# Kernel optimization log

Measured on AMD Instinct MI355X. Metric: run time of the kernel, lower is better.

## Reference

```python
import jax, jax.numpy as jnp
import numpy as np

B, T_IN, T_OUT = 64, 512, 500
N_MEL, ENC_DIM, ATT_DIM = 80, 512, 128
ATT_RNN, DEC_RNN, PRENET = 1024, 1024, 256
N_FILT, KSIZE = 32, 31
PAD = (KSIZE - 1) // 2


def setup_inputs() -> dict:
    key = jax.random.key(0)
    ks = jax.random.split(key, 20)
    g = lambda i, shape, s: jax.random.normal(ks[i], shape, jnp.float32) * s
    return {
        'memory': g(0, (B, T_IN, ENC_DIM), 1.0),
        'decoder_inputs': g(1, (B, N_MEL, T_OUT), 1.0),
        'memory_lengths': jax.random.randint(ks[2], (B,), T_IN // 2, T_IN + 1).astype(jnp.int32),
        'prenet_w1': g(3, (PRENET, N_MEL), 0.05),
        'prenet_w2': g(4, (PRENET, PRENET), 0.05),
        'att_wih': g(5, (4 * ATT_RNN, PRENET + ENC_DIM), 0.02),
        'att_whh': g(6, (4 * ATT_RNN, ATT_RNN), 0.02),
        'att_bih': jnp.zeros((4 * ATT_RNN,), jnp.float32),
        'att_bhh': jnp.zeros((4 * ATT_RNN,), jnp.float32),
        'wq': g(7, (ATT_DIM, ATT_RNN), 0.03),
        'wm': g(8, (ATT_DIM, ENC_DIM), 0.03),
        'v': g(9, (ATT_DIM,), 0.05),
        'loc_conv': g(10, (N_FILT, 2, KSIZE), 0.05),
        'loc_dense': g(11, (ATT_DIM, N_FILT), 0.05),
        'dec_wih': g(12, (4 * DEC_RNN, ATT_RNN + ENC_DIM), 0.02),
        'dec_whh': g(13, (4 * DEC_RNN, DEC_RNN), 0.02),
        'dec_bih': jnp.zeros((4 * DEC_RNN,), jnp.float32),
        'dec_bhh': jnp.zeros((4 * DEC_RNN,), jnp.float32),
        'proj_w': g(14, (N_MEL, DEC_RNN + ENC_DIM), 0.02),
        'proj_b': jnp.zeros((N_MEL,), jnp.float32),
        'gate_w': g(15, (1, DEC_RNN + ENC_DIM), 0.02),
        'gate_b': jnp.zeros((1,), jnp.float32),
    }


def _lstm_cell(x, h, c, wih, whh, bih, bhh):
    gates = x @ wih.T + bih + h @ whh.T + bhh
    i, f, g, o = jnp.split(gates, 4, axis=-1)
    c_new = jax.nn.sigmoid(f) * c + jax.nn.sigmoid(i) * jnp.tanh(g)
    h_new = jax.nn.sigmoid(o) * jnp.tanh(c_new)
    return h_new, c_new


def _forward(memory, decoder_inputs, memory_lengths, prenet_w1, prenet_w2,
             att_wih, att_whh, att_bih, att_bhh, wq, wm, v, loc_conv, loc_dense,
             dec_wih, dec_whh, dec_bih, dec_bhh, proj_w, proj_b, gate_w, gate_b):
    # padding mask: True at padded encoder positions
    mask = jnp.arange(T_IN)[None, :] >= memory_lengths[:, None]  # [B, T_in]
    processed_memory = memory @ wm.T  # [B, T_in, ATT_DIM]

    # parse decoder inputs -> [T_out, B, N_MEL]; prepend all-zero go frame
    di = jnp.transpose(decoder_inputs, (2, 0, 1))
    di = jnp.concatenate([jnp.zeros((1, B, N_MEL), di.dtype), di], axis=0)

    # prenet (dropout p=0.5 is always active in the original; deterministic key)
    dk1, dk2 = jax.random.split(jax.random.key(42))
    x = jax.nn.relu(di @ prenet_w1.T)
    x = x * jax.random.bernoulli(dk1, 0.5, x.shape).astype(x.dtype) * 2.0
    x = jax.nn.relu(x @ prenet_w2.T)
    x = x * jax.random.bernoulli(dk2, 0.5, x.shape).astype(x.dtype) * 2.0  # [T_out+1, B, PRENET]

    def step(carry, x_t):
        ah, ac, dh, dc, aw, awc, ctx = carry
        # attention LSTM
        ah, ac = _lstm_cell(jnp.concatenate([x_t, ctx], -1), ah, ac,
                            att_wih, att_whh, att_bih, att_bhh)
        # location-sensitive attention
        awcat = jnp.stack([aw, awc], axis=1)  # [B, 2, T_in]
        loc = jax.lax.conv_general_dilated(awcat, loc_conv, (1,), [(PAD, PAD)],
                                           dimension_numbers=('NCH', 'OIH', 'NCH'))  # [B, F, T_in]
        loc = jnp.einsum('bft,af->bta', loc, loc_dense)  # [B, T_in, ATT_DIM]
        pq = (ah @ wq.T)[:, None, :]  # [B, 1, ATT_DIM]
        energies = jnp.tanh(pq + loc + processed_memory) @ v  # [B, T_in]
        energies = jnp.where(mask, -jnp.inf, energies)
        aw = jax.nn.softmax(energies, axis=1)
        ctx = jnp.einsum('bt,btd->bd', aw, memory)
        awc = awc + aw
        # decoder LSTM
        dh, dc = _lstm_cell(jnp.concatenate([ah, ctx], -1), dh, dc,
                            dec_wih, dec_whh, dec_bih, dec_bhh)
        dhc = jnp.concatenate([dh, ctx], -1)  # [B, DEC_RNN+ENC_DIM]
        mel = dhc @ proj_w.T + proj_b  # [B, N_MEL]
        gate = (dhc @ gate_w.T + gate_b)[:, 0]  # [B]
        return (ah, ac, dh, dc, aw, awc, ctx), (mel, gate, aw)

    z = lambda *s: jnp.zeros(s, jnp.float32)
    init = (z(B, ATT_RNN), z(B, ATT_RNN), z(B, DEC_RNN), z(B, DEC_RNN),
            z(B, T_IN), z(B, T_IN), z(B, ENC_DIM))
    _, (mels, gates, aws) = jax.lax.scan(step, init, x[:T_OUT])
    mel_outputs = jnp.transpose(mels, (1, 0, 2)).reshape(B, -1, N_MEL)  # [B, T_out, N_MEL]
    gate_outputs = gates.T  # [B, T_out]
    alignments = jnp.transpose(aws, (1, 0, 2))  # [B, T_out, T_in]
    return mel_outputs, gate_outputs, alignments


def reference(memory, decoder_inputs, memory_lengths, prenet_w1, prenet_w2,
              att_wih, att_whh, att_bih, att_bhh, wq, wm, v, loc_conv, loc_dense,
              dec_wih, dec_whh, dec_bih, dec_bhh, proj_w, proj_b, gate_w, gate_b):
    return _forward(memory, decoder_inputs, memory_lengths, prenet_w1, prenet_w2,
                    att_wih, att_whh, att_bih, att_bhh, wq, wm, v, loc_conv, loc_dense,
                    dec_wih, dec_whh, dec_bih, dec_bhh, proj_w, proj_b, gate_w, gate_b)
```

## Files before the change

kernel.cpp:

```cpp
#include <hip/hip_runtime.h>
#include <cstdint>
#include <cstddef>

#define NB    64
#define TIN   512
#define TOUT  500
#define NMEL  80
#define ENC   512
#define ATTD  128
#define ARNN  1024
#define DRNN  1024
#define PREN  256
#define NFILT 32
#define KSZ   31
#define CPAD  15

#define MEL_OFF  0
#define GATE_OFF 2560000
#define ALGN_OFF 2592000

#define X_SZ      8192000
#define PM_SZ     4194304
#define G1_SZ     1048576
#define G2_SZ     1048576
#define XATT_SZ   98304
#define XDEC_SZ   163840
#define AC_SZ     65536
#define DC_SZ     65536
#define AW_SZ     32768
#define AWC_SZ    32768
#define TAILH_SZ  49152
#define TAILL_SZ  49152
#define XDH_SZ    81920
#define XDL_SZ    81920
#define PQ_SZ     8192
#define EN_SZ     32768
#define MASK_N    8208384

#define K1TOT   1792
#define K2TOT   2560
#define NCH1    56
#define NCH2    80
#define PK1_N   14680064
#define PK2_N   20971520

typedef unsigned short u16;
typedef __attribute__((ext_vector_type(8))) short bf16x8;
typedef __attribute__((ext_vector_type(4))) float f32x4;

__device__ __forceinline__ uint32_t rotl32(uint32_t v, int r) { return (v << r) | (v >> (32 - r)); }

__device__ __forceinline__ float sigf(float x) { return 1.f / (1.f + __expf(-x)); }
__device__ __forceinline__ float tanhf_fast(float x) {
    float ax = fabsf(x);
    float t = 1.f - 2.f / (__expf(2.f * ax) + 1.f);
    return copysignf(t, x);
}

__device__ __forceinline__ void split1(float v, u16& h, u16& l) {
    uint32_t u = __float_as_uint(v);
    h = (u16)(u >> 16);
    float r = v - __uint_as_float(u & 0xFFFF0000u);
    uint32_t ru = __float_as_uint(r);
    ru += 0x7FFFu + ((ru >> 16) & 1u);
    l = (u16)(ru >> 16);
}

__device__ __forceinline__ void split8(float4 f0, float4 f1, bf16x8& h, bf16x8& l) {
    float v[8] = { f0.x, f0.y, f0.z, f0.w, f1.x, f1.y, f1.z, f1.w };
#pragma unroll
    for (int i = 0; i < 8; ++i) {
        uint32_t u = __float_as_uint(v[i]);
        h[i] = (short)(u >> 16);
        float r = v[i] - __uint_as_float(u & 0xFFFF0000u);
        uint32_t ru = __float_as_uint(r);
        ru += 0x7FFFu + ((ru >> 16) & 1u);
        l[i] = (short)(ru >> 16);
    }
}

#define MFMA16(a, b, c) __builtin_amdgcn_mfma_f32_16x16x32_bf16(a, b, c, 0, 0, 0)

__device__ void tf_block(uint32_t k1, uint32_t k2, uint32_t& x0, uint32_t& x1) {
    uint32_t ks0 = k1, ks1 = k2, ks2 = k1 ^ k2 ^ 0x1BD11BDAu;
    x0 += ks0; x1 += ks1;
#define TFR(r) { x0 += x1; x1 = rotl32(x1, r); x1 ^= x0; }
    TFR(13) TFR(15) TFR(26) TFR(6)   x0 += ks1; x1 += ks2 + 1u;
    TFR(17) TFR(29) TFR(16) TFR(24)  x0 += ks2; x1 += ks0 + 2u;
    TFR(13) TFR(15) TFR(26) TFR(6)   x0 += ks0; x1 += ks1 + 3u;
    TFR(17) TFR(29) TFR(16) TFR(24)  x0 += ks1; x1 += ks2 + 4u;
    TFR(13) TFR(15) TFR(26) TFR(6)   x0 += ks2; x1 += ks0 + 5u;
#undef TFR
}

__global__ __launch_bounds__(256) void mask_kernel(unsigned char* m1, unsigned char* m2) {
    int i = blockIdx.x * 256 + threadIdx.x;
    if (i >= MASK_N) return;
    uint32_t a0 = 0u, a1 = 0u; tf_block(0u, 42u, a0, a1);
    uint32_t b0 = 0u, b1 = 1u; tf_block(0u, 42u, b0, b1);
    uint32_t x0, x1;
    x0 = 0u; x1 = (uint32_t)i; tf_block(a0, a1, x0, x1);
    m1[i] = ((x0 ^ x1) >> 31) == 0u;
    x0 = 0u; x1 = (uint32_t)i; tf_block(b0, b1, x0, x1);
    m2[i] = ((x0 ^ x1) >> 31) == 0u;
}

__global__ __launch_bounds__(256) void prenet1_kernel(
    const float* __restrict__ dec_in, const float* __restrict__ w1,
    const unsigned char* __restrict__ m1, float* __restrict__ x)
{
    int r = blockIdx.x;
    int t = r >> 6, b = r & 63;
    int tid = threadIdx.x;
    __shared__ float ds[NMEL];
    if (tid < NMEL) ds[tid] = (t == 0) ? 0.f : dec_in[(size_t)b * 40000 + tid * 500 + (t - 1)];
    __syncthreads();
    float acc = 0.f;
    const float* w = w1 + tid * NMEL;
#pragma unroll
    for (int k = 0; k < NMEL; ++k) acc += ds[k] * w[k];
    acc = fmaxf(acc, 0.f);
    int flat = r * 256 + tid;
    x[flat] = m1[flat] ? acc * 2.f : 0.f;
}

__global__ __launch_bounds__(256) void prenet2_kernel(
    const float* __restrict__ w2, const unsigned char* __restrict__ m2, float* x)
{
    int r = blockIdx.x;
    int tid = threadIdx.x;
    __shared__ float xs[PREN];
    xs[tid] = x[r * 256 + tid];
    __syncthreads();
    float acc = 0.f;
    const float* w = w2 + tid * PREN;
#pragma unroll 8
    for (int k = 0; k < PREN; ++k) acc += xs[k] * w[k];
    acc = fmaxf(acc, 0.f);
    int flat = r * 256 + tid;
    x[flat] = m2[flat] ? acc * 2.f : 0.f;
}

__global__ __launch_bounds__(128) void pm_kernel(
    const float* __restrict__ memory, const float* __restrict__ wm, float* __restrict__ pm)
{
    int b = blockIdx.x, t = blockIdx.y;
    int tid = threadIdx.x;
    __shared__ float ms[ENC];
    for (int i = tid; i < ENC; i += 128) ms[i] = memory[(size_t)b * (TIN * ENC) + (size_t)t * ENC + i];
    __syncthreads();
    float acc = 0.f;
    const float* w = wm + tid * ENC;
#pragma unroll 8
    for (int k = 0; k < ENC; ++k) acc += ms[k] * w[k];
    pm[(size_t)b * (TIN * ATTD) + t * ATTD + tid] = acc;
}

__global__ __launch_bounds__(256) void wpack_kernel(
    const float* __restrict__ w1, int K1, const float* __restrict__ w2, int K2,
    u16* __restrict__ dst)
{
    const int K = K1 + K2;
    int idx = blockIdx.x * 256 + threadIdx.x;
    if (idx >= 4096 * K) return;
    int n = idx / K, k = idx % K;
    float v = (k < K1) ? w1[n * K1 + k] : w2[n * K2 + (k - K1)];
    u16 h, l;
    split1(v, h, l);
    int tile = n >> 4, kc = k >> 5;
    int lane = (n & 15) + (((k & 31) >> 3) << 4);
    size_t off = ((size_t)(tile * (K >> 5) + kc) * 2) * 512 + lane * 8 + (k & 7);
    dst[off] = h;
    dst[off + 512] = l;
}

struct SmemGemm { float Xs[32][68]; float Ws[32][68]; };

__device__ void gemm_phase(
    const float* __restrict__ X1, int ldx1, int kx1,
    const float* __restrict__ X2, int ldx2,
    const float* __restrict__ W1, int ldw1, int kw1,
    const float* __restrict__ W2, int ldw2,
    float* __restrict__ outp, int Kq, int blk, SmemGemm& s)
{
    const int tid = threadIdx.x;
    const int n0 = (blk & 63) * 64;
    const int ks = blk >> 6;
    const int kbeg = ks * Kq;
    const int tn = tid & 15, tm = tid >> 4;
    float acc[4][4];
#pragma unroll
    for (int i = 0; i < 4; ++i)
#pragma unroll
        for (int j = 0; j < 4; ++j) acc[i][j] = 0.f;

#pragma unroll 1
    for (int k0 = kbeg; k0 < kbeg + Kq; k0 += 32) {
#pragma unroll
        for (int i = 0; i < 8; ++i) {
            int flat = i * 256 + tid;
            int m = flat >> 5, c = flat & 31;
            int k = k0 + c;
            s.Xs[c][m] = (k < kx1) ? X1[m * ldx1 + k] : X2[m * ldx2 + (k - kx1)];
        }
#pragma unroll
        for (int i = 0; i < 8; ++i) {
            int flat = i * 256 + tid;
            int r = flat >> 5, c = flat & 31;
            int k = k0 + c;
            int n = n0 + r;
            s.Ws[c][r] = (k < kw1) ? W1[n * ldw1 + k] : W2[n * ldw2 + (k - kw1)];
        }
        __syncthreads();
#pragma unroll
        for (int kk = 0; kk < 32; ++kk) {
            float4 xv = *(const float4*)&s.Xs[kk][tm * 4];
            float4 wv = *(const float4*)&s.Ws[kk][tn * 4];
            float xr[4] = { xv.x, xv.y, xv.z, xv.w };
            float wr[4] = { wv.x, wv.y, wv.z, wv.w };
#pragma unroll
            for (int i = 0; i < 4; ++i)
#pragma unroll
                for (int j = 0; j < 4; ++j) acc[i][j] += xr[i] * wr[j];
        }
        __syncthreads();
    }
    float* o = outp + (size_t)ks * 64 * 4096;
#pragma unroll
    for (int i = 0; i < 4; ++i)
#pragma unroll
        for (int j = 0; j < 4; ++j)
            o[(tm * 4 + i) * 4096 + (n0 + tn * 4 + j)] = acc[i][j];
}

__global__ __launch_bounds__(256, 2) void pair_gemm(
    const float* __restrict__ xcat_dec,
    const float* __restrict__ dec_wih, const float* __restrict__ dec_whh,
    float* __restrict__ g2,
    const float* __restrict__ x, const float* __restrict__ xcat_att,
    const float* __restrict__ att_wih, const float* __restrict__ att_whh,
    float* __restrict__ g1, int t)
{
    __shared__ __align__(16) SmemGemm sm;
    const int blk = blockIdx.x;
    if (blk < 256) {
        if (t < 0) return;
        gemm_phase(xcat_dec, 2560, 2560, xcat_dec, 2560,
                   dec_wih, 1536, 1536, dec_whh, 1024, g2, 640, blk, sm);
    } else {
        const int tn = t + 1;
        if (tn >= TOUT) return;
        gemm_phase(x + (size_t)tn * (NB * PREN), PREN, PREN, xcat_att, 1536,
                   att_wih, 768, 768, att_whh, 1024, g1, 448, blk - 256, sm);
    }
}

__global__ __launch_bounds__(256) void mfma_pair_gemm(
    const u16* __restrict__ xdech, const u16* __restrict__ xdecl,
    const u16* __restrict__ pk2, float* __restrict__ g2,
    const float* __restrict__ x,
    const u16* __restrict__ tailh, const u16* __restrict__ taill,
    const u16* __restrict__ pk1, float* __restrict__ g1, int t)
{
    const int blk = blockIdx.x;
    const int tid = threadIdx.x;
    const int wave = tid >> 6, lane = tid & 63;
    const int lr = lane & 15, kg = lane >> 4;
    const int mrow = wave * 16 + lr;
    f32x4 acc = {0.f, 0.f, 0.f, 0.f};

    if (blk < 512) {
        if (t < 0) return;
        const int tile = blk >> 1, ks = blk & 1;
        const int c_beg = ks * (NCH2 / 2), c_end = c_beg + NCH2 / 2;
        const u16* Ah = xdech + mrow * 2560;
        const u16* Al = xdecl + mrow * 2560;
        const u16* bp = pk2 + (size_t)tile * NCH2 * 1024 + lane * 8;
#pragma unroll 4
        for (int kc = c_beg; kc < c_end; ++kc) {
            const int k = kc * 32 + kg * 8;
            bf16x8 ah = *(const bf16x8*)(Ah + k);
            bf16x8 al = *(const bf16x8*)(Al + k);
            const u16* c0 = bp + (size_t)kc * 1024;
            bf16x8 bh = *(const bf16x8*)c0;
            bf16x8 bl = *(const bf16x8*)(c0 + 512);
            acc = MFMA16(ah, bh, acc); acc = MFMA16(ah, bl, acc); acc = MFMA16(al, bh, acc);
        }
        const int n0 = tile * 16;
        const int mbase = wave * 16 + kg * 4;
        float* o = g2 + (size_t)ks * 262144;
#pragma unroll
        for (int r = 0; r < 4; ++r)
            o[(mbase + r) * 4096 + n0 + lr] = acc[r];
    } else {
        const int tn = t + 1;
        if (tn >= TOUT) return;
        const int bb = blk - 512;
        const int tile = bb >> 1, ks = bb & 1;
        const int c_beg = ks * (NCH1 / 2), c_end = c_beg + NCH1 / 2;
        const u16* Ah = tailh + mrow * 1536;
        const u16* Al = taill + mrow * 1536;
        const float* xr = x + ((size_t)tn * 64 + mrow) * 256;
        const u16* bp = pk1 + (size_t)tile * NCH1 * 1024 + lane * 8;
#pragma unroll 4
        for (int kc = c_beg; kc < c_end; ++kc) {
            const int k = kc * 32 + kg * 8;
            bf16x8 ah, al;
            if (k < 256) {
                float4 f0 = *(const float4*)(xr + k);
                float4 f1 = *(const float4*)(xr + k + 4);
                split8(f0, f1, ah, al);
            } else {
                ah = *(const bf16x8*)(Ah + (k - 256));
                al = *(const bf16x8*)(Al + (k - 256));
            }
            const u16* c0 = bp + (size_t)kc * 1024;
            bf16x8 bh = *(const bf16x8*)c0;
            bf16x8 bl = *(const bf16x8*)(c0 + 512);
            acc = MFMA16(ah, bh, acc); acc = MFMA16(ah, bl, acc); acc = MFMA16(al, bh, acc);
        }
        const int n0 = tile * 16;
        const int mbase = wave * 16 + kg * 4;
        float* o = g1 + (size_t)ks * 262144;
#pragma unroll
        for (int r = 0; r < 4; ++r)
            o[(mbase + r) * 4096 + n0 + lr] = acc[r];
    }
}

__global__ __launch_bounds__(256) void pair_pw(
    const float* __restrict__ g1, const float* __restrict__ att_bih, const float* __restrict__ att_bhh,
    float* __restrict__ ac, float* __restrict__ xcat_att, float* __restrict__ xcat_dec,
    const float* __restrict__ wq, float* __restrict__ pq,
    const float* __restrict__ g2, const float* __restrict__ dec_bih, const float* __restrict__ dec_bhh,
    float* __restrict__ dc, const float* __restrict__ proj_w, const float* __restrict__ proj_b,
    const float* __restrict__ gate_w, const float* __restrict__ gate_b,
    float* __restrict__ out,
    u16* __restrict__ tailh, u16* __restrict__ taill,
    u16* __restrict__ xdech, u16* __restrict__ xdecl,
    int nsplit, int t)
{
    const int tid = threadIdx.x;
    __shared__ float sbuf[1536];
    __shared__ float red[256];

    if (blockIdx.x < 64) {
        if (t >= TOUT) return;
        const int b = blockIdx.x;
#pragma unroll
        for (int q = 0; q < 4; ++q) {
            int j = q * 256 + tid;
            float gi = att_bih[j] + att_bhh[j];
            float gf = att_bih[1024 + j] + att_bhh[1024 + j];
            float gg = att_bih[2048 + j] + att_bhh[2048 + j];
            float go = att_bih[3072 + j] + att_bhh[3072 + j];
            for (int s = 0; s < nsplit; ++s) {
                const float* g = g1 + (size_t)s * 262144 + b * 4096;
                gi += g[j]; gf += g[1024 + j]; gg += g[2048 + j]; go += g[3072 + j];
            }
            float c = sigf(gf) * ac[b * 1024 + j] + sigf(gi) * tanhf_fast(gg);
            float h = sigf(go) * tanhf_fast(c);
            ac[b * 1024 + j] = c;
            xcat_att[b * 1536 + 512 + j] = h;
            xcat_dec[b * 2560 + j] = h;
            u16 hh, hl; split1(h, hh, hl);
            tailh[b * 1536 + 512 + j] = hh;  taill[b * 1536 + 512 + j] = hl;
            xdech[b * 2560 + j] = hh;        xdecl[b * 2560 + j] = hl;
            sbuf[j] = h;
        }
        __syncthreads();
        const int a = tid & 127, half = tid >> 7;
        const float* wr = wq + a * 1024 + half * 512;
        const float* hh = sbuf + half * 512;
        float s0 = 0.f, s1 = 0.f, s2 = 0.f, s3 = 0.f;
#pragma unroll 4
        for (int k = 0; k < 512; k += 16) {
            float4 w0 = *(const float4*)&wr[k],      h0 = *(const float4*)&hh[k];
            float4 w1 = *(const float4*)&wr[k + 4],  h1 = *(const float4*)&hh[k + 4];
            float4 w2 = *(const float4*)&wr[k + 8],  h2 = *(const float4*)&hh[k + 8];
            float4 w3 = *(const float4*)&wr[k + 12], h3 = *(const float4*)&hh[k + 12];
            s0 += h0.x * w0.x + h0.y * w0.y + h0.z * w0.z + h0.w * w0.w;
            s1 += h1.x * w1.x + h1.y * w1.y + h1.z * w1.z + h1.w * w1.w;
            s2 += h2.x * w2.x + h2.y * w2.y + h2.z * w2.z + h2.w * w2.w;
            s3 += h3.x * w3.x + h3.y * w3.y + h3.z * w3.z + h3.w * w3.w;
        }
        red[tid] = (s0 + s1) + (s2 + s3);
        __syncthreads();
        if (half == 0) pq[b * 128 + a] = red[a] + red[a + 128];
    } else {
        if (t < 1) return;
        const int b = blockIdx.x - 64;
        const int ts = t - 1;
#pragma unroll
        for (int q = 0; q < 4; ++q) {
            int j = q * 256 + tid;
            float gi = dec_bih[j] + dec_bhh[j];
            float gf = dec_bih[1024 + j] + dec_bhh[1024 + j];
            float gg = dec_bih[2048 + j] + dec_bhh[2048 + j];
            float go = dec_bih[3072 + j] + dec_bhh[3072 + j];
            for (int s = 0; s < nsplit; ++s) {
                const float* g = g2 + (size_t)s * 262144 + b * 4096;
                gi += g[j]; gf += g[1024 + j]; gg += g[2048 + j]; go += g[3072 + j];
            }
            float c = sigf(gf) * dc[b * 1024 + j] + sigf(gi) * tanhf_fast(gg);
            float h = sigf(go) * tanhf_fast(c);
            dc[b * 1024 + j] = c;
            xcat_dec[b * 2560 + 1536 + j] = h;
            u16 hh, hl; split1(h, hh, hl);
            xdech[b * 2560 + 1536 + j] = hh;  xdecl[b * 2560 + 1536 + j] = hl;
            sbuf[j] = h;
        }
        for (int i = tid; i < 512; i += 256) sbuf[1024 + i] = xcat_dec[b * 2560 + 1024 + i];
        __syncthreads();
        const int o = tid >> 1, half = tid & 1;
        float accv = 0.f;
        if (o <= 80) {
            const float* w = (o < 80) ? (proj_w + o * 1536) : gate_w;
            const float* sv = sbuf + half * 768;
            const float* wv = w + half * 768;
            float s0 = 0.f, s1 = 0.f, s2 = 0.f, s3 = 0.f;
#pragma unroll 4
            for (int k = 0; k < 768; k += 16) {
                float4 a0 = *(const float4*)&sv[k],      b0 = *(const float4*)&wv[k];
                float4 a1 = *(const float4*)&sv[k + 4],  b1 = *(const float4*)&wv[k + 4];
                float4 a2 = *(const float4*)&sv[k + 8],  b2 = *(const float4*)&wv[k + 8];
                float4 a3 = *(const float4*)&sv[k + 12], b3 = *(const float4*)&wv[k + 12];
                s0 += a0.x * b0.x + a0.y * b0.y + a0.z * b0.z + a0.w * b0.w;
                s1 += a1.x * b1.x + a1.y * b1.y + a1.z * b1.z + a1.w * b1.w;
                s2 += a2.x * b2.x + a2.y * b2.y + a2.z * b2.z + a2.w * b2.w;
                s3 += a3.x * b3.x + a3.y * b3.y + a3.z * b3.z + a3.w * b3.w;
            }
            accv = (s0 + s1) + (s2 + s3);
        }
        red[tid] = accv;
        __syncthreads();
        if (half == 0 && o <= 80) {
            float r = red[tid] + red[tid + 1];
            if (o < 80)
                out[MEL_OFF + (size_t)b * (TOUT * NMEL) + (size_t)ts * NMEL + o] = r + proj_b[o];
            else
                out[GATE_OFF + (size_t)b * TOUT + ts] = r + gate_b[0];
        }
    }
}

__global__ __launch_bounds__(256) void energies_kernel(
    const float* __restrict__ aw, const float* __restrict__ awc,
    const float* __restrict__ lc, const float* __restrict__ ld,
    const float* __restrict__ vvec, const float* __restrict__ pq,
    const float* __restrict__ pm, float* __restrict__ energ)
{
    const int b = blockIdx.x, tc = blockIdx.y;
    const int t0 = tc * 64;
    const int tid = threadIdx.x;
    __shared__ float awin[96], awcin[96];
    __shared__ float lcs[NFILT * 62];
    __shared__ float locs[64 * 33];
    __shared__ float pqs[ATTD], vs[ATTD];
    __shared__ float ldm[ATTD * 33];

    for (int i = tid; i < 94; i += 256) {
        int t = t0 + i - CPAD;
        bool ok = (t >= 0 && t < TIN);
        awin[i]  = ok ? aw[b * TIN + t]  : 0.f;
        awcin[i] = ok ? awc[b * TIN + t] : 0.f;
    }
    for (int i = tid; i < NFILT * 62; i += 256) lcs[i] = lc[i];
    for (int i = tid; i < ATTD * NFILT; i += 256) ldm[(i >> 5) * 33 + (i & 31)] = ld[i];
    if (tid < ATTD) { pqs[tid] = pq[b * ATTD + tid]; vs[tid] = vvec[tid]; }
    __syncthreads();

    for (int idx = tid; idx < 64 * 32; idx += 256) {
        int tl = idx >> 5, f = idx & 31;
        const float* w0 = lcs + f * 62;
        float s = 0.f;
#pragma unroll
        for (int k = 0; k < KSZ; ++k)
            s += awin[tl + k] * w0[k] + awcin[tl + k] * w0[31 + k];
        locs[tl * 33 + f] = s;
    }
    __syncthreads();

    const int tl = tid >> 2, q = tid & 3;
    const int a0 = q * 32;
    const float* pmrow = pm + (size_t)b * (TIN * ATTD) + (size_t)(t0 + tl) * ATTD + a0;
    const float* lt = locs + tl * 33;
    float4 pv[8];
#pragma unroll
    for (int u = 0; u < 8; ++u) pv[u] = *(const float4*)&pmrow[u * 4];
    float e = 0.f;
#pragma unroll
    for (int aa = 0; aa < 32; ++aa) {
        int a = a0 + aa;
        float sv = pqs[a] + ((const float*)pv)[aa];
        const float* lrow = ldm + a * 33;
#pragma unroll
        for (int f = 0; f < NFILT; ++f) sv += lt[f] * lrow[f];
        e += vs[a] * tanhf_fast(sv);
    }
    e += __shfl_xor(e, 1);
    e += __shfl_xor(e, 2);
    if (q == 0) energ[b * TIN + t0 + tl] = e;
}

__global__ __launch_bounds__(256) void softmax_ctx_kernel(
    const float* __restrict__ energ, const int* __restrict__ mlen,
    const float* __restrict__ memory,
    float* __restrict__ aw, float* __restrict__ awc,
    float* __restrict__ out_align, int t_step,
    float* __restrict__ xcat_att, float* __restrict__ xcat_dec,
    u16* __restrict__ tailh, u16* __restrict__ taill,
    u16* __restrict__ xdech, u16* __restrict__ xdecl)
{
    const int b = blockIdx.x >> 3, dq = blockIdx.x & 7;
    const int tid = threadIdx.x;
    const int len = mlen[b];
    __shared__ float es[TIN];
    __shared__ float red[256];

    float e1 = (tid < len) ? energ[b * TIN + tid] : -INFINITY;
    float e2 = (tid + 256 < len) ? energ[b * TIN + tid + 256] : -INFINITY;
    red[tid] = fmaxf(e1, e2);
    __syncthreads();
    for (int s = 128; s > 0; s >>= 1) {
        if (tid < s) red[tid] = fmaxf(red[tid], red[tid + s]);
        __syncthreads();
    }
    const float mx = red[0];
    __syncthreads();
    float p1 = __expf(e1 - mx);
    float p2 = __expf(e2 - mx);
    red[tid] = p1 + p2;
    __syncthreads();
    for (int s = 128; s > 0; s >>= 1) {
        if (tid < s) red[tid] += red[tid + s];
        __syncthreads();
    }
    const float inv = 1.f / red[0];
    p1 *= inv; p2 *= inv;
    es[tid] = p1; es[tid + 256] = p2;
    __syncthreads();

    if (tid < 64) {
        int tt = dq * 64 + tid;
        float p = es[tt];
        aw[b * TIN + tt] = p;
        awc[b * TIN + tt] += p;
        out_align[(size_t)b * (TOUT * TIN) + (size_t)t_step * TIN + tt] = p;
    }

    const int d = dq * 64 + (tid & 63), th = tid >> 6;
    const float* mb = memory + (size_t)b * (TIN * ENC);
    float accv = 0.f;
#pragma unroll 4
    for (int tt = th * 128; tt < th * 128 + 128; ++tt)
        accv += es[tt] * mb[(size_t)tt * ENC + d];
    red[tid] = accv;
    __syncthreads();
    if (tid < 64) {
        float cv = (red[tid] + red[tid + 64]) + (red[tid + 128] + red[tid + 192]);
        int dd = dq * 64 + tid;
        xcat_att[b * 1536 + dd] = cv;
        xcat_dec[b * 2560 + 1024 + dd] = cv;
        u16 h, l; split1(cv, h, l);
        tailh[b * 1536 + dd] = h;        taill[b * 1536 + dd] = l;
        xdech[b * 2560 + 1024 + dd] = h; xdecl[b * 2560 + 1024 + dd] = l;
    }
}

extern "C" void kernel_launch(void* const* d_in, const int* in_sizes, int n_in,
                              void* d_out, int out_size, void* d_ws, size_t ws_size,
                              hipStream_t stream) {
    const float* memory   = (const float*)d_in[0];
    const float* dec_in   = (const float*)d_in[1];
    const int*   mlen     = (const int*)d_in[2];
    const float* pw1      = (const float*)d_in[3];
    const float* pw2      = (const float*)d_in[4];
    const float* att_wih  = (const float*)d_in[5];
    const float* att_whh  = (const float*)d_in[6];
    const float* att_bih  = (const float*)d_in[7];
    const float* att_bhh  = (const float*)d_in[8];
    const float* wq       = (const float*)d_in[9];
    const float* wm       = (const float*)d_in[10];
    const float* v        = (const float*)d_in[11];
    const float* loc_conv = (const float*)d_in[12];
    const float* loc_dense= (const float*)d_in[13];
    const float* dec_wih  = (const float*)d_in[14];
    const float* dec_whh  = (const float*)d_in[15];
    const float* dec_bih  = (const float*)d_in[16];
    const float* dec_bhh  = (const float*)d_in[17];
    const float* proj_w   = (const float*)d_in[18];
    const float* proj_b   = (const float*)d_in[19];
    const float* gate_w   = (const float*)d_in[20];
    const float* gate_b   = (const float*)d_in[21];
    float* out = (float*)d_out;

    float* x        = (float*)d_ws;
    float* pm       = x + X_SZ;
    float* g1       = pm + PM_SZ;
    float* g2       = g1 + G1_SZ;
    float* xcat_att = g2 + G2_SZ;
    float* xcat_dec = xcat_att + XATT_SZ;
    float* ac       = xcat_dec + XDEC_SZ;
    float* dc       = ac + AC_SZ;
    float* aw       = dc + DC_SZ;
    float* awc      = aw + AW_SZ;
    float* tailh_f  = awc + AWC_SZ;
    float* taill_f  = tailh_f + TAILH_SZ;
    float* xdech_f  = taill_f + TAILL_SZ;
    float* xdecl_f  = xdech_f + XDH_SZ;
    float* pq       = xdecl_f + XDL_SZ;
    float* energ    = pq + PQ_SZ;
    unsigned char* m1 = (unsigned char*)(energ + EN_SZ);
    unsigned char* m2 = m1 + MASK_N;
    u16* pk1 = (u16*)(m2 + MASK_N);
    u16* pk2 = pk1 + PK1_N;

    u16* tailh = (u16*)tailh_f;  u16* taill = (u16*)taill_f;
    u16* xdech = (u16*)xdech_f;  u16* xdecl = (u16*)xdecl_f;

    size_t need_base = (size_t)(m2 + MASK_N - (unsigned char*)d_ws);
    size_t need_full = (size_t)((unsigned char*)(pk2 + PK2_N) - (unsigned char*)d_ws);
    if (ws_size < need_base) return;
    const bool use_mfma = (ws_size >= need_full);
    const int nsplit = use_mfma ? 2 : 4;

    size_t state_floats = (size_t)XATT_SZ + XDEC_SZ + AC_SZ + DC_SZ + AW_SZ + AWC_SZ
                        + TAILH_SZ + TAILL_SZ + XDH_SZ + XDL_SZ;
    hipMemsetAsync(xcat_att, 0, state_floats * sizeof(float), stream);

    mask_kernel<<<(MASK_N + 255) / 256, 256, 0, stream>>>(m1, m2);
    prenet1_kernel<<<TOUT * NB, 256, 0, stream>>>(dec_in, pw1, m1, x);
    prenet2_kernel<<<TOUT * NB, 256, 0, stream>>>(pw2, m2, x);
    pm_kernel<<<dim3(NB, TIN), 128, 0, stream>>>(memory, wm, pm);
    if (use_mfma) {
        wpack_kernel<<<(4096 * K1TOT + 255) / 256, 256, 0, stream>>>(att_wih, 768, att_whh, 1024, pk1);
        wpack_kernel<<<(4096 * K2TOT + 255) / 256, 256, 0, stream>>>(dec_wih, 1536, dec_whh, 1024, pk2);
    }

    float* out_align = out + ALGN_OFF;

    if (use_mfma)
        mfma_pair_gemm<<<1024, 256, 0, stream>>>(xdech, xdecl, pk2, g2, x, tailh, taill, pk1, g1, -1);
    else
        pair_gemm<<<512, 256, 0, stream>>>(xcat_dec, dec_wih, dec_whh, g2,
                                           x, xcat_att, att_wih, att_whh, g1, -1);

    for (int t = 0; t < TOUT; ++t) {
        pair_pw<<<128, 256, 0, stream>>>(g1, att_bih, att_bhh, ac, xcat_att, xcat_dec, wq, pq,
                                         g2, dec_bih, dec_bhh, dc, proj_w, proj_b,
                                         gate_w, gate_b, out, tailh, taill, xdech, xdecl,
                                         nsplit, t);
        energies_kernel<<<dim3(NB, 8), 256, 0, stream>>>(aw, awc, loc_conv, loc_dense, v, pq, pm, energ);
        softmax_ctx_kernel<<<512, 256, 0, stream>>>(energ, mlen, memory, aw, awc, out_align, t,
                                                    xcat_att, xcat_dec, tailh, taill, xdech, xdecl);
        if (use_mfma)
            mfma_pair_gemm<<<1024, 256, 0, stream>>>(xdech, xdecl, pk2, g2, x, tailh, taill, pk1, g1, t);
        else
            pair_gemm<<<512, 256, 0, stream>>>(xcat_dec, dec_wih, dec_whh, g2,
                                               x, xcat_att, att_wih, att_whh, g1, t);
    }
    pair_pw<<<128, 256, 0, stream>>>(g1, att_bih, att_bhh, ac, xcat_att, xcat_dec, wq, pq,
                                     g2, dec_bih, dec_bhh, dc, proj_w, proj_b,
                                     gate_w, gate_b, out, tailh, taill, xdech, xdecl,
                                     nsplit, TOUT);
}
```

Baseline: 61.15 ms.

## Overlap energies with partial LSTM GEMMs and split K into early/late phases

Splits each LSTM gate GEMM's K range into three parts. The K chunks whose inputs (dec hidden, att hidden, prenet x) are already known before softmax/context are computed in a fused kernel that also runs the attention energies blocks concurrently. Only the context-dependent chunks run after softmax_ctx in a smaller late GEMM. This hides GEMM work behind the energies stage and shortens the serial tail after softmax, but it adds a third partial-sum buffer (nsplit=3) that the pointwise kernel must reduce, plus extra modulo indexing in the K loop.

```diff
diff --git a/kernel.cpp b/kernel.cpp
--- a/kernel.cpp
+++ b/kernel.cpp
@@ -255,7 +255,108 @@
     }
 }
 
-__global__ __launch_bounds__(256) void mfma_pair_gemm(
+__device__ __forceinline__ void mfma_tile_run(
+    const u16* __restrict__ Ah, const u16* __restrict__ Al, int aoff,
+    const float* __restrict__ xr,
+    const u16* __restrict__ bp, int kc_beg, int nchunk, int kc_wrap_at, int kc_wrap_to,
+    f32x4& acc, int lane)
+{
+    const int kg = lane >> 4;
+#pragma unroll 4
+    for (int i = 0; i < nchunk; ++i) {
+        int kc = kc_beg + i;
+        if (kc >= kc_wrap_at) kc = kc_wrap_to + (kc - kc_wrap_at);
+        const int k = kc * 32 + kg * 8;
+        bf16x8 ah, al;
+        if (xr && k < 256) {
+            float4 f0 = *(const float4*)(xr + k);
+            float4 f1 = *(const float4*)(xr + k + 4);
+            split8(f0, f1, ah, al);
+        } else {
+            ah = *(const bf16x8*)(Ah + (k - aoff));
+            al = *(const bf16x8*)(Al + (k - aoff));
+        }
+        const u16* c0 = bp + (size_t)kc * 1024;
+        bf16x8 bh = *(const bf16x8*)c0;
+        bf16x8 bl = *(const bf16x8*)(c0 + 512);
+        acc = MFMA16(ah, bh, acc); acc = MFMA16(ah, bl, acc); acc = MFMA16(al, bh, acc);
+    }
+}
+
+__device__ __forceinline__ void mfma_store(float* o, f32x4 acc, int tile, int wave, int lane)
+{
+    const int n0 = tile * 16;
+    const int mbase = wave * 16 + (lane >> 4) * 4;
+    const int lr = lane & 15;
+#pragma unroll
+    for (int r = 0; r < 4; ++r)
+        o[(mbase + r) * 4096 + n0 + lr] = acc[r];
+}
+
+__device__ void energies_body(
+    int b, int tc,
+    const float* __restrict__ aw, const float* __restrict__ awc,
+    const float* __restrict__ lc, const float* __restrict__ ld,
+    const float* __restrict__ vvec, const float* __restrict__ pq,
+    const float* __restrict__ pm, float* __restrict__ energ)
+{
+    const int t0 = tc * 64;
+    const int tid = threadIdx.x;
+    __shared__ float awin[96], awcin[96];
+    __shared__ float lcs[NFILT * 62];
+    __shared__ float locs[64 * 33];
+    __shared__ float pqs[ATTD], vs[ATTD];
+    __shared__ float ldm[ATTD * 33];
+
+    for (int i = tid; i < 94; i += 256) {
+        int t = t0 + i - CPAD;
+        bool ok = (t >= 0 && t < TIN);
+        awin[i]  = ok ? aw[b * TIN + t]  : 0.f;
+        awcin[i] = ok ? awc[b * TIN + t] : 0.f;
+    }
+    for (int i = tid; i < NFILT * 62; i += 256) lcs[i] = lc[i];
+    for (int i = tid; i < ATTD * NFILT; i += 256) ldm[(i >> 5) * 33 + (i & 31)] = ld[i];
+    if (tid < ATTD) { pqs[tid] = pq[b * ATTD + tid]; vs[tid] = vvec[tid]; }
+    __syncthreads();
+
+    for (int idx = tid; idx < 64 * 32; idx += 256) {
+        int tl = idx >> 5, f = idx & 31;
+        const float* w0 = lcs + f * 62;
+        float s = 0.f;
+#pragma unroll
+        for (int k = 0; k < KSZ; ++k)
+            s += awin[tl + k] * w0[k] + awcin[tl + k] * w0[31 + k];
+        locs[tl * 33 + f] = s;
+    }
+    __syncthreads();
+
+    const int tl = tid >> 2, q = tid & 3;
+    const int a0 = q * 32;
+    const float* pmrow = pm + (size_t)b * (TIN * ATTD) + (size_t)(t0 + tl) * ATTD + a0;
+    const float* lt = locs + tl * 33;
+    float4 pv[8];
+#pragma unroll
+    for (int u = 0; u < 8; ++u) pv[u] = *(const float4*)&pmrow[u * 4];
+    float e = 0.f;
+#pragma unroll
+    for (int aa = 0; aa < 32; ++aa) {
+        int a = a0 + aa;
+        float sv = pqs[a] + ((const float*)pv)[aa];
+        const float* lrow = ldm + a * 33;
+#pragma unroll
+        for (int f = 0; f < NFILT; ++f) sv += lt[f] * lrow[f];
+        e += vs[a] * tanhf_fast(sv);
+    }
+    e += __shfl_xor(e, 1);
+    e += __shfl_xor(e, 2);
+    if (q == 0) energ[b * TIN + t0 + tl] = e;
+}
+
+__global__ __launch_bounds__(256) void fused_mid(
+    const float* __restrict__ aw, const float* __restrict__ awc,
+    const float* __restrict__ lc, const float* __restrict__ ld,
+    const float* __restrict__ vvec, const float* __restrict__ pq,
+    const float* __restrict__ pm, float* __restrict__ energ,
     const u16* __restrict__ xdech, const u16* __restrict__ xdecl,
     const u16* __restrict__ pk2, float* __restrict__ g2,
     const float* __restrict__ x,
@@ -263,68 +364,64 @@
     const u16* __restrict__ pk1, float* __restrict__ g1, int t)
 {
     const int blk = blockIdx.x;
+    if (blk < 512) {
+        if (t < 0) return;
+        energies_body(blk >> 3, blk & 7, aw, awc, lc, ld, vvec, pq, pm, energ);
+        return;
+    }
     const int tid = threadIdx.x;
     const int wave = tid >> 6, lane = tid & 63;
-    const int lr = lane & 15, kg = lane >> 4;
-    const int mrow = wave * 16 + lr;
+    const int mrow = wave * 16 + (lane & 15);
     f32x4 acc = {0.f, 0.f, 0.f, 0.f};
 
-    if (blk < 512) {
+    if (blk < 1024) {
         if (t < 0) return;
-        const int tile = blk >> 1, ks = blk & 1;
-        const int c_beg = ks * (NCH2 / 2), c_end = c_beg + NCH2 / 2;
-        const u16* Ah = xdech + mrow * 2560;
-        const u16* Al = xdecl + mrow * 2560;
+        const int r = blk - 512;
+        const int tile = r & 255, ks = r >> 8;
         const u16* bp = pk2 + (size_t)tile * NCH2 * 1024 + lane * 8;
-#pragma unroll 4
-        for (int kc = c_beg; kc < c_end; ++kc) {
-            const int k = kc * 32 + kg * 8;
-            bf16x8 ah = *(const bf16x8*)(Ah + k);
-            bf16x8 al = *(const bf16x8*)(Al + k);
-            const u16* c0 = bp + (size_t)kc * 1024;
-            bf16x8 bh = *(const bf16x8*)c0;
-            bf16x8 bl = *(const bf16x8*)(c0 + 512);
-            acc = MFMA16(ah, bh, acc); acc = MFMA16(ah, bl, acc); acc = MFMA16(al, bh, acc);
-        }
-        const int n0 = tile * 16;
-        const int mbase = wave * 16 + kg * 4;
-        float* o = g2 + (size_t)ks * 262144;
-#pragma unroll
-        for (int r = 0; r < 4; ++r)
-            o[(mbase + r) * 4096 + n0 + lr] = acc[r];
+        mfma_tile_run(xdech + mrow * 2560, xdecl + mrow * 2560, 0, nullptr,
+                      bp, ks == 0 ? 0 : 48, 32, 1000, 0, acc, lane);
+        mfma_store(g2 + (size_t)ks * 262144, acc, tile, wave, lane);
     } else {
         const int tn = t + 1;
         if (tn >= TOUT) return;
-        const int bb = blk - 512;
-        const int tile = bb >> 1, ks = bb & 1;
-        const int c_beg = ks * (NCH1 / 2), c_end = c_beg + NCH1 / 2;
-        const u16* Ah = tailh + mrow * 1536;
-        const u16* Al = taill + mrow * 1536;
+        const int r = blk - 1024;
+        const int tile = r & 255, ks = r >> 8;
+        const u16* bp = pk1 + (size_t)tile * NCH1 * 1024 + lane * 8;
         const float* xr = x + ((size_t)tn * 64 + mrow) * 256;
+        mfma_tile_run(tailh + mrow * 1536, taill + mrow * 1536, 256, xr,
+                      bp, ks == 0 ? 24 : 44, 20, 56, 0, acc, lane);
+        mfma_store(g1 + (size_t)ks * 262144, acc, tile, wave, lane);
+    }
+}
+
+__global__ __launch_bounds__(256) void gemm_late(
+    const u16* __restrict__ xdech, const u16* __restrict__ xdecl,
+    const u16* __restrict__ pk2, float* __restrict__ g2,
+    const u16* __restrict__ tailh, const u16* __restrict__ taill,
+    const u16* __restrict__ pk1, float* __restrict__ g1, int t)
+{
+    const int blk = blockIdx.x;
+    const int tid = threadIdx.x;
+    const int wave = tid >> 6, lane = tid & 63;
+    const int mrow = wave * 16 + (lane & 15);
+    f32x4 acc = {0.f, 0.f, 0.f, 0.f};
+
+    if (blk < 256) {
+        if (t < 0) return;
+        const int tile = blk;
+        const u16* bp = pk2 + (size_t)tile * NCH2 * 1024 + lane * 8;
+        mfma_tile_run(xdech + mrow * 2560, xdecl + mrow * 2560, 0, nullptr,
+                      bp, 32, 16, 1000, 0, acc, lane);
+        mfma_store(g2 + (size_t)2 * 262144, acc, tile, wave, lane);
+    } else {
+        const int tn = t + 1;
+        if (tn >= TOUT) return;
+        const int tile = blk - 256;
         const u16* bp = pk1 + (size_t)tile * NCH1 * 1024 + lane * 8;
-#pragma unroll 4
-        for (int kc = c_beg; kc < c_end; ++kc) {
-            const int k = kc * 32 + kg * 8;
-            bf16x8 ah, al;
-            if (k < 256) {
-                float4 f0 = *(const float4*)(xr + k);
-                float4 f1 = *(const float4*)(xr + k + 4);
-                split8(f0, f1, ah, al);
-            } else {
-                ah = *(const bf16x8*)(Ah + (k - 256));
-                al = *(const bf16x8*)(Al + (k - 256));
-            }
-            const u16* c0 = bp + (size_t)kc * 1024;
-            bf16x8 bh = *(const bf16x8*)c0;
-            bf16x8 bl = *(const bf16x8*)(c0 + 512);
-            acc = MFMA16(ah, bh, acc); acc = MFMA16(ah, bl, acc); acc = MFMA16(al, bh, acc);
-        }
-        const int n0 = tile * 16;
-        const int mbase = wave * 16 + kg * 4;
-        float* o = g1 + (size_t)ks * 262144;
-#pragma unroll
-        for (int r = 0; r < 4; ++r)
-            o[(mbase + r) * 4096 + n0 + lr] = acc[r];
+        mfma_tile_run(tailh + mrow * 1536, taill + mrow * 1536, 256, nullptr,
+                      bp, 8, 16, 1000, 0, acc, lane);
+        mfma_store(g1 + (size_t)2 * 262144, acc, tile, wave, lane);
     }
 }
 
@@ -450,57 +547,7 @@
     const float* __restrict__ vvec, const float* __restrict__ pq,
     const float* __restrict__ pm, float* __restrict__ energ)
 {
-    const int b = blockIdx.x, tc = blockIdx.y;
-    const int t0 = tc * 64;
-    const int tid = threadIdx.x;
-    __shared__ float awin[96], awcin[96];
-    __shared__ float lcs[NFILT * 62];
-    __shared__ float locs[64 * 33];
-    __shared__ float pqs[ATTD], vs[ATTD];
-    __shared__ float ldm[ATTD * 33];
-
-    for (int i = tid; i < 94; i += 256) {
-        int t = t0 + i - CPAD;
-        bool ok = (t >= 0 && t < TIN);
-        awin[i]  = ok ? aw[b * TIN + t]  : 0.f;
-        awcin[i] = ok ? awc[b * TIN + t] : 0.f;
-    }
-    for (int i = tid; i < NFILT * 62; i += 256) lcs[i] = lc[i];
-    for (int i = tid; i < ATTD * NFILT; i += 256) ldm[(i >> 5) * 33 + (i & 31)] = ld[i];
-    if (tid < ATTD) { pqs[tid] = pq[b * ATTD + tid]; vs[tid] = vvec[tid]; }
-    __syncthreads();
-
-    for (int idx = tid; idx < 64 * 32; idx += 256) {
-        int tl = idx >> 5, f = idx & 31;
-        const float* w0 = lcs + f * 62;
-        float s = 0.f;
-#pragma unroll
-        for (int k = 0; k < KSZ; ++k)
-            s += awin[tl + k] * w0[k] + awcin[tl + k] * w0[31 + k];
-        locs[tl * 33 + f] = s;
-    }
-    __syncthreads();
-
-    const int tl = tid >> 2, q = tid & 3;
-    const int a0 = q * 32;
-    const float* pmrow = pm + (size_t)b * (TIN * ATTD) + (size_t)(t0 + tl) * ATTD + a0;
-    const float* lt = locs + tl * 33;
-    float4 pv[8];
-#pragma unroll
-    for (int u = 0; u < 8; ++u) pv[u] = *(const float4*)&pmrow[u * 4];
-    float e = 0.f;
-#pragma unroll
-    for (int aa = 0; aa < 32; ++aa) {
-        int a = a0 + aa;
-        float sv = pqs[a] + ((const float*)pv)[aa];
-        const float* lrow = ldm + a * 33;
-#pragma unroll
-        for (int f = 0; f < NFILT; ++f) sv += lt[f] * lrow[f];
-        e += vs[a] * tanhf_fast(sv);
-    }
-    e += __shfl_xor(e, 1);
-    e += __shfl_xor(e, 2);
-    if (q == 0) energ[b * TIN + t0 + tl] = e;
+    energies_body(blockIdx.x >> 3, blockIdx.x & 7, aw, awc, lc, ld, vvec, pq, pm, energ);
 }
 
 __global__ __launch_bounds__(256) void softmax_ctx_kernel(
@@ -623,7 +670,7 @@
     size_t need_full = (size_t)((unsigned char*)(pk2 + PK2_N) - (unsigned char*)d_ws);
     if (ws_size < need_base) return;
     const bool use_mfma = (ws_size >= need_full);
-    const int nsplit = use_mfma ? 2 : 4;
+    const int nsplit = use_mfma ? 3 : 4;
 
     size_t state_floats = (size_t)XATT_SZ + XDEC_SZ + AC_SZ + DC_SZ + AW_SZ + AWC_SZ
                         + TAILH_SZ + TAILL_SZ + XDH_SZ + XDL_SZ;
@@ -640,25 +687,33 @@
 
     float* out_align = out + ALGN_OFF;
 
-    if (use_mfma)
-        mfma_pair_gemm<<<1024, 256, 0, stream>>>(xdech, xdecl, pk2, g2, x, tailh, taill, pk1, g1, -1);
-    else
+    if (use_mfma) {
+        fused_mid<<<1536, 256, 0, stream>>>(aw, awc, loc_conv, loc_dense, v, pq, pm, energ,
+                                            xdech, xdecl, pk2, g2, x, tailh, taill, pk1, g1, -1);
+        gemm_late<<<512, 256, 0, stream>>>(xdech, xdecl, pk2, g2, tailh, taill, pk1, g1, -1);
+    } else {
         pair_gemm<<<512, 256, 0, stream>>>(xcat_dec, dec_wih, dec_whh, g2,
                                            x, xcat_att, att_wih, att_whh, g1, -1);
+    }
 
     for (int t = 0; t < TOUT; ++t) {
         pair_pw<<<128, 256, 0, stream>>>(g1, att_bih, att_bhh, ac, xcat_att, xcat_dec, wq, pq,
                                          g2, dec_bih, dec_bhh, dc, proj_w, proj_b,
                                          gate_w, gate_b, out, tailh, taill, xdech, xdecl,
                                          nsplit, t);
-        energies_kernel<<<dim3(NB, 8), 256, 0, stream>>>(aw, awc, loc_conv, loc_dense, v, pq, pm, energ);
-        softmax_ctx_kernel<<<512, 256, 0, stream>>>(energ, mlen, memory, aw, awc, out_align, t,
-                                                    xcat_att, xcat_dec, tailh, taill, xdech, xdecl);
-        if (use_mfma)
-            mfma_pair_gemm<<<1024, 256, 0, stream>>>(xdech, xdecl, pk2, g2, x, tailh, taill, pk1, g1, t);
-        else
+        if (use_mfma) {
+            fused_mid<<<1536, 256, 0, stream>>>(aw, awc, loc_conv, loc_dense, v, pq, pm, energ,
+                                                xdech, xdecl, pk2, g2, x, tailh, taill, pk1, g1, t);
+            softmax_ctx_kernel<<<512, 256, 0, stream>>>(energ, mlen, memory, aw, awc, out_align, t,
+                                                        xcat_att, xcat_dec, tailh, taill, xdech, xdecl);
+            gemm_late<<<512, 256, 0, stream>>>(xdech, xdecl, pk2, g2, tailh, taill, pk1, g1, t);
+        } else {
+            energies_kernel<<<512, 256, 0, stream>>>(aw, awc, loc_conv, loc_dense, v, pq, pm, energ);
+            softmax_ctx_kernel<<<512, 256, 0, stream>>>(energ, mlen, memory, aw, awc, out_align, t,
+                                                        xcat_att, xcat_dec, tailh, taill, xdech, xdecl);
             pair_gemm<<<512, 256, 0, stream>>>(xcat_dec, dec_wih, dec_whh, g2,
                                                x, xcat_att, att_wih, att_whh, g1, t);
+        }
     }
     pair_pw<<<128, 256, 0, stream>>>(g1, att_bih, att_bhh, ac, xcat_att, xcat_dec, wq, pq,
                                      g2, dec_bih, dec_bhh, dc, proj_w, proj_b,
```

New measurement: 53.88 ms. 1.13x faster.
